# Optimization experiments

Hardware: AMD Instinct MI355X
Metric: run time of the kernel (lower is better)

Reference implementation:

```python
import jax, jax.numpy as jnp
import numpy as np

EMBED_DIM = 768
NUM_HEADS = 12
HEAD_DIM = EMBED_DIM // NUM_HEADS


def setup_inputs() -> dict:
    key = jax.random.key(0)
    k1, k2, k3, k4, k5 = jax.random.split(key, 5)
    x_q = jax.random.normal(k1, (8, 1024, EMBED_DIM), dtype=jnp.float32)
    s = 1.0 / np.sqrt(EMBED_DIM)
    qkv_w = jax.random.uniform(k2, (3 * EMBED_DIM, EMBED_DIM), jnp.float32, -s, s)
    qkv_b = jax.random.uniform(k3, (3 * EMBED_DIM,), jnp.float32, -s, s)
    out_w = jax.random.uniform(k4, (EMBED_DIM, EMBED_DIM), jnp.float32, -s, s)
    out_b = jax.random.uniform(k5, (EMBED_DIM,), jnp.float32, -s, s)
    return {"x_q": x_q, "qkv_w": qkv_w, "qkv_b": qkv_b, "out_w": out_w, "out_b": out_b}


def reference(x_q, qkv_w, qkv_b, out_w, out_b):
    b, p, c = x_q.shape
    scaling = HEAD_DIM ** (-0.5)
    # qkv projection: [b, p, 3c]
    qkv = x_q @ qkv_w.T + qkv_b
    qkv = qkv.reshape(b, p, 3, NUM_HEADS, HEAD_DIM)
    q = qkv[:, :, 0].transpose(0, 2, 1, 3) * scaling  # [b, h, p, d]
    k = qkv[:, :, 1].transpose(0, 2, 1, 3)
    v = qkv[:, :, 2].transpose(0, 2, 1, 3)
    attn = jnp.einsum('bhqd,bhkd->bhqk', q, k)
    attn = jax.nn.softmax(attn, axis=-1)
    out = jnp.einsum('bhqk,bhkd->bhqd', attn, v)
    out = out.transpose(0, 2, 1, 3).reshape(b, p, c)
    return out @ out_w.T + out_b
```

## Files before the change

kernel.cpp:

```cpp
#include <hip/hip_runtime.h>
#include <stdint.h>

typedef float  f32x4 __attribute__((ext_vector_type(4)));
typedef int    i32x4 __attribute__((ext_vector_type(4)));
typedef short  bf16x8 __attribute__((ext_vector_type(8)));
typedef unsigned short u16;
typedef unsigned int   u32;

#define DEVINL __device__ __forceinline__

DEVINL u16 f2bf(float f) {
  u32 u = __builtin_bit_cast(u32, f);
  u32 r = u + 0x7fffu + ((u >> 16) & 1u);
  return (u16)(r >> 16);
}

DEVINL u32 cvtpk(float lo, float hi) {
  u32 r;
  asm("v_cvt_pk_bf16_f32 %0, %1, %2" : "=v"(r) : "v"(lo), "v"(hi));
  return r;
}

DEVINL void mfma16(f32x4& d, i32x4 a, i32x4 b) {
  d = __builtin_amdgcn_mfma_f32_16x16x32_bf16(
      __builtin_bit_cast(bf16x8, a), __builtin_bit_cast(bf16x8, b), d, 0, 0, 0);
}

#define GLD16(gp, lp) __builtin_amdgcn_global_load_lds( \
    (__attribute__((address_space(1))) void*)(gp), \
    (__attribute__((address_space(3))) void*)(lp), 16, 0, 0)

__global__ void cvt3_f32_bf16(const float* __restrict__ s0, u16* __restrict__ d0, int n0,
                              const float* __restrict__ s1, u16* __restrict__ d1, int n1,
                              const float* __restrict__ s2, u16* __restrict__ d2, int n2) {
  int i = blockIdx.x * blockDim.x + threadIdx.x;
  int stride = gridDim.x * blockDim.x;
  int nt = n0 + n1 + n2;
  for (; i < nt; i += stride) {
    const float* s; u16* d; int j = i;
    if (j < n0) { s = s0; d = d0; }
    else if ((j -= n0) < n1) { s = s1; d = d1; }
    else { j -= n1; s = s2; d = d2; }
    float4 v = ((const float4*)s)[j];
    ushort4 o;
    o.x = f2bf(v.x); o.y = f2bf(v.y); o.z = f2bf(v.z); o.w = f2bf(v.w);
    ((ushort4*)d)[j] = o;
  }
}

template<int BM, int BN, int FM, int FN, int EPI>
__global__ __launch_bounds__(256) void gemm_bt(
    const u16* __restrict__ A, const u16* __restrict__ Bw,
    int M, int N, const float* __restrict__ bias,
    float* __restrict__ Cf, u16* __restrict__ Qb, u16* __restrict__ Kb, u16* __restrict__ Vtb)
{
  constexpr int BK = 32;
  constexpr int K  = 768;
  constexpr int ABYT = BM * BK * 2;
  constexpr int BBYT = BN * BK * 2;
  __shared__ __align__(16) unsigned char sm[2 * (ABYT + BBYT)];

  const int tid = threadIdx.x;
  const int l   = tid & 63;
  const int wid = tid >> 6;
  const int wm  = wid >> 1, wn = wid & 1;
  const int g4  = l >> 4;
  const int c15 = l & 15;

  const int ntiles = N / BN;
  const int wg  = ntiles * (M / BM);
  const int per = wg >> 3;
  const int tile = ((int)blockIdx.x & 7) * per + ((int)blockIdx.x >> 3);
  const int mbase = (tile / ntiles) * BM;
  const int nbase = (tile % ntiles) * BN;

  auto stage = [&](int buf, int kt) {
    unsigned char* ab = sm + buf * (ABYT + BBYT);
    unsigned char* bb = ab + ABYT;
    #pragma unroll
    for (int c = 0; c < BM / 64; ++c) {
      int ch = c * 256 + tid;
      int row = ch & (BM - 1), pl = ch / BM;
      GLD16(A + (size_t)(mbase + row) * K + kt * BK + pl * 8, ab + ch * 16);
    }
    #pragma unroll
    for (int c = 0; c < BN / 64; ++c) {
      int ch = c * 256 + tid;
      int row = ch & (BN - 1), pl = ch / BN;
      GLD16(Bw + (size_t)(nbase + row) * K + kt * BK + pl * 8, bb + ch * 16);
    }
  };

  f32x4 acc[FM][FN] = {};

  stage(0, 0);
  __syncthreads();

  for (int kt = 0; kt < K / BK; ++kt) {
    int cur = kt & 1;
    if (kt + 1 < K / BK) stage(cur ^ 1, kt + 1);
    unsigned char* ab = sm + cur * (ABYT + BBYT);
    unsigned char* bb = ab + ABYT;
    i32x4 af[FM], bf[FN];
    #pragma unroll
    for (int mt = 0; mt < FM; ++mt) {
      int row = wm * (BM / 2) + mt * 16 + c15;
      af[mt] = *(const i32x4*)(ab + (g4 * BM + row) * 16);
    }
    #pragma unroll
    for (int nt = 0; nt < FN; ++nt) {
      int row = wn * (BN / 2) + nt * 16 + c15;
      bf[nt] = *(const i32x4*)(bb + (g4 * BN + row) * 16);
    }
    __builtin_amdgcn_s_setprio(1);
    #pragma unroll
    for (int mt = 0; mt < FM; ++mt)
      #pragma unroll
      for (int nt = 0; nt < FN; ++nt)
        mfma16(acc[mt][nt], af[mt], bf[nt]);
    __builtin_amdgcn_s_setprio(0);
    __syncthreads();
  }

  if constexpr (EPI == 0) {
    #pragma unroll
    for (int nt = 0; nt < FN; ++nt) {
      int n = nbase + wn * (BN / 2) + nt * 16 + c15;
      float bv = bias[n];
      #pragma unroll
      for (int mt = 0; mt < FM; ++mt) {
        int m0 = mbase + wm * (BM / 2) + mt * 16 + g4 * 4;
        float* dst = Cf + (size_t)m0 * N + n;
        #pragma unroll
        for (int j = 0; j < 4; ++j) dst[(size_t)j * N] = acc[mt][nt][j] + bv;
      }
    }
  } else {
    #pragma unroll
    for (int nt = 0; nt < FN; ++nt) {
      int n = nbase + wn * (BN / 2) + nt * 16 + c15;
      int which = n / 768;
      int rem = n - which * 768;
      int h = rem >> 6, d = rem & 63;
      float bv = bias[n];
      #pragma unroll
      for (int mt = 0; mt < FM; ++mt) {
        int m0 = mbase + wm * (BM / 2) + mt * 16 + g4 * 4;
        int b = m0 >> 10, p0 = m0 & 1023;
        int bh = b * 12 + h;
        if (which == 0) {
          u16* dst = Qb + ((size_t)bh * 1024 + p0) * 64 + d;
          #pragma unroll
          for (int j = 0; j < 4; ++j) dst[(size_t)j * 64] = f2bf((acc[mt][nt][j] + bv) * 0.125f);
        } else if (which == 1) {
          u16* dst = Kb + ((size_t)bh * 1024 + p0) * 64 + d;
          #pragma unroll
          for (int j = 0; j < 4; ++j) dst[(size_t)j * 64] = f2bf(acc[mt][nt][j] + bv);
        } else {
          uint2 uu;
          uu.x = cvtpk(acc[mt][nt][0] + bv, acc[mt][nt][1] + bv);
          uu.y = cvtpk(acc[mt][nt][2] + bv, acc[mt][nt][3] + bv);
          *(uint2*)(Vtb + ((size_t)bh * 64 + d) * 1024 + p0) = uu;
        }
      }
    }
  }
}

__global__ __launch_bounds__(256) void attn_fwd(
    const u16* __restrict__ Qb, const u16* __restrict__ Kb,
    const u16* __restrict__ Vtb, u16* __restrict__ Ob)
{
  __shared__ __align__(16) unsigned char sm[16384 + 4 * 8192];
  const int tid = threadIdx.x;
  const int l = tid & 63, wid = tid >> 6;
  const int g4 = l >> 4, c15 = l & 15;
  const int bid = blockIdx.x;
  const int bh = bid % 96, qt = bid / 96;

  const size_t bhoff = (size_t)bh * (1024 * 64);
  const u16* Qg = Qb + bhoff + (size_t)qt * 128 * 64;
  const u16* Kg = Kb + bhoff;
  const u16* Vg = Vtb + bhoff;

  #pragma unroll
  for (int c = 0; c < 4; ++c) {
    int ch = c * 256 + tid;
    int row = ch & 127, pl = ch >> 7;
    GLD16(Qg + (size_t)row * 64 + pl * 8, sm + ch * 16);
  }

  auto stageKV = [&](int buf, int t) {
    unsigned char* kb_ = sm + 16384 + buf * 8192;
    unsigned char* vb_ = sm + 32768 + buf * 8192;
    #pragma unroll
    for (int c = 0; c < 2; ++c) {
      int ch = c * 256 + tid;
      int row = ch & 63, pl = ch >> 6;
      GLD16(Kg + (size_t)(t * 64 + row) * 64 + pl * 8, kb_ + ch * 16);
      GLD16(Vg + (size_t)row * 1024 + t * 64 + pl * 8, vb_ + ch * 16);
    }
  };

  stageKV(0, 0);
  __syncthreads();

  i32x4 qf[2][2];
  #pragma unroll
  for (int qn = 0; qn < 2; ++qn)
    #pragma unroll
    for (int ks = 0; ks < 2; ++ks) {
      int row = wid * 32 + qn * 16 + c15;
      qf[qn][ks] = *(const i32x4*)(sm + ((ks * 4 + g4) * 128 + row) * 16);
    }
  __syncthreads();

  unsigned char* pw = sm + wid * 4096;

  const i32x4 ones = {0x3F803F80, 0x3F803F80, 0x3F803F80, 0x3F803F80};
  constexpr float LOG2E = 1.44269504f;

  f32x4 ot[4][2] = {};
  f32x4 lacc[2] = {};
  float mrow[2] = {-1e30f, -1e30f};
  float mc[2]   = {-1e30f, -1e30f};

  for (int t = 0; t < 16; ++t) {
    int cur = t & 1;
    if (t + 1 < 16) stageKV(cur ^ 1, t + 1);
    unsigned char* kb_ = sm + 16384 + cur * 8192;
    unsigned char* vb_ = sm + 32768 + cur * 8192;

    f32x4 st[4][2] = {};
    __builtin_amdgcn_s_setprio(1);
    #pragma unroll
    for (int ks = 0; ks < 2; ++ks)
      #pragma unroll
      for (int kmt = 0; kmt < 4; ++kmt) {
        i32x4 ka = *(const i32x4*)(kb_ + ((ks * 4 + g4) * 64 + kmt * 16 + c15) * 16);
        mfma16(st[kmt][0], ka, qf[0][ks]);
        mfma16(st[kmt][1], ka, qf[1][ks]);
      }
    __builtin_amdgcn_s_setprio(0);

    #pragma unroll
    for (int qn = 0; qn < 2; ++qn) {
      float mx = fmaxf(fmaxf(fmaxf(st[0][qn][0], st[0][qn][1]), fmaxf(st[0][qn][2], st[0][qn][3])),
                       fmaxf(fmaxf(st[1][qn][0], st[1][qn][1]), fmaxf(st[1][qn][2], st[1][qn][3])));
      mx = fmaxf(mx,
           fmaxf(fmaxf(fmaxf(st[2][qn][0], st[2][qn][1]), fmaxf(st[2][qn][2], st[2][qn][3])),
                 fmaxf(fmaxf(st[3][qn][0], st[3][qn][1]), fmaxf(st[3][qn][2], st[3][qn][3]))));
      mx = fmaxf(mx, __shfl_xor(mx, 16));
      mx = fmaxf(mx, __shfl_xor(mx, 32));
      if (!__all(mx - mrow[qn] <= 8.0f)) {
        float mnew = fmaxf(mrow[qn], mx);
        float sfq = exp2f((mrow[qn] - mnew) * LOG2E);
        mrow[qn] = mnew;
        mc[qn] = mnew * LOG2E;
        #pragma unroll
        for (int dmt = 0; dmt < 4; ++dmt)
          #pragma unroll
          for (int j = 0; j < 4; ++j) ot[dmt][qn][j] *= sfq;
        lacc[qn][0] *= sfq;
      }
      #pragma unroll
      for (int kmt = 0; kmt < 4; ++kmt) {
        float p0 = exp2f(__builtin_fmaf(st[kmt][qn][0], LOG2E, -mc[qn]));
        float p1 = exp2f(__builtin_fmaf(st[kmt][qn][1], LOG2E, -mc[qn]));
        float p2 = exp2f(__builtin_fmaf(st[kmt][qn][2], LOG2E, -mc[qn]));
        float p3 = exp2f(__builtin_fmaf(st[kmt][qn][3], LOG2E, -mc[qn]));
        int k0 = kmt * 16 + 4 * g4;
        uint2 ww;
        ww.x = cvtpk(p0, p1);
        ww.y = cvtpk(p2, p3);
        *(uint2*)(pw + ((k0 >> 3) * 32 + qn * 16 + c15) * 16 + (k0 & 7) * 2) = ww;
      }
    }

    i32x4 pb[2][2];
    #pragma unroll
    for (int qn = 0; qn < 2; ++qn)
      #pragma unroll
      for (int ks = 0; ks < 2; ++ks)
        pb[qn][ks] = *(const i32x4*)(pw + (((ks * 4 + g4) * 32) + qn * 16 + c15) * 16);

    __builtin_amdgcn_s_setprio(1);
    #pragma unroll
    for (int ks = 0; ks < 2; ++ks) {
      #pragma unroll
      for (int dmt = 0; dmt < 4; ++dmt) {
        i32x4 va = *(const i32x4*)(vb_ + ((ks * 4 + g4) * 64 + dmt * 16 + c15) * 16);
        mfma16(ot[dmt][0], va, pb[0][ks]);
        mfma16(ot[dmt][1], va, pb[1][ks]);
      }
      mfma16(lacc[0], ones, pb[0][ks]);
      mfma16(lacc[1], ones, pb[1][ks]);
    }
    __builtin_amdgcn_s_setprio(0);
    __syncthreads();
  }

  const int b = bh / 12, h = bh % 12;
  #pragma unroll
  for (int qn = 0; qn < 2; ++qn) {
    float inv = 1.0f / lacc[qn][0];
    int q = qt * 128 + wid * 32 + qn * 16 + c15;
    size_t rowoff = ((size_t)(b * 1024 + q) * 12 + h) * 64;
    #pragma unroll
    for (int dmt = 0; dmt < 4; ++dmt) {
      int d0 = dmt * 16 + g4 * 4;
      uint2 uu;
      uu.x = cvtpk(ot[dmt][qn][0] * inv, ot[dmt][qn][1] * inv);
      uu.y = cvtpk(ot[dmt][qn][2] * inv, ot[dmt][qn][3] * inv);
      *(uint2*)(Ob + rowoff + d0) = uu;
    }
  }
}

extern "C" void kernel_launch(void* const* d_in, const int* in_sizes, int n_in,
                              void* d_out, int out_size, void* d_ws, size_t ws_size,
                              hipStream_t stream) {
  const float* x    = (const float*)d_in[0];
  const float* qkvw = (const float*)d_in[1];
  const float* qkvb = (const float*)d_in[2];
  const float* outw = (const float*)d_in[3];
  const float* outb = (const float*)d_in[4];
  float* out = (float*)d_out;

  unsigned char* ws = (unsigned char*)d_ws;
  u16* xb  = (u16*)(ws);
  u16* wqb = (u16*)(ws + 12582912);
  u16* wob = (u16*)(ws + 16121856);
  u16* Qbf = (u16*)(ws + 17301504);
  u16* Kbf = (u16*)(ws + 29884416);
  u16* Vtb = (u16*)(ws + 42467328);
  u16* Ob  = xb;

  cvt3_f32_bf16<<<dim3(2048), dim3(256), 0, stream>>>(
      x, xb, 8192 * 768 / 4, qkvw, wqb, 2304 * 768 / 4, outw, wob, 768 * 768 / 4);

  gemm_bt<128, 128, 4, 4, 1><<<dim3(1152), dim3(256), 0, stream>>>(
      xb, wqb, 8192, 2304, qkvb, nullptr, Qbf, Kbf, Vtb);

  attn_fwd<<<dim3(768), dim3(256), 0, stream>>>(Qbf, Kbf, Vtb, Ob);

  gemm_bt<128, 64, 4, 2, 0><<<dim3(768), dim3(256), 0, stream>>>(
      Ob, wob, 8192, 768, outb, out, nullptr, nullptr, nullptr);
}
```

Before: 175.7 us.

## Replace QKV GEMM with 256x256-tile 8-wave kernel and split-phase pipeline

Replaces the 128x128 QKV projection GEMM with a dedicated 512-thread kernel that computes 256x256 output tiles using BK=64, double-buffered 128KB LDS, and a four-phase schedule per k-step. Each phase interleaves register loads from LDS, half-tile async prefetches of the next step and MFMA bursts, using explicit barriers and vmcnt waits. The larger tile raises arithmetic intensity and cuts global reloads of A and B. The cost is one block per CU with 288 blocks on 256 CUs, which leaves a partial second wave, plus high register pressure from 128 accumulator floats per thread. The output-projection GEMM template drops its unused QKV epilogue.

```diff
diff --git a/kernel.cpp b/kernel.cpp
--- a/kernel.cpp
+++ b/kernel.cpp
@@ -29,6 +29,10 @@
 #define GLD16(gp, lp) __builtin_amdgcn_global_load_lds( \
     (__attribute__((address_space(1))) void*)(gp), \
     (__attribute__((address_space(3))) void*)(lp), 16, 0, 0)
+
+#define VMW(n) do { asm volatile("s_waitcnt vmcnt(" #n ")" ::: "memory"); \
+                    __builtin_amdgcn_sched_barrier(0); } while (0)
+#define BAR() __builtin_amdgcn_s_barrier()
 
 __global__ void cvt3_f32_bf16(const float* __restrict__ s0, u16* __restrict__ d0, int n0,
                               const float* __restrict__ s1, u16* __restrict__ d1, int n1,
@@ -48,11 +52,176 @@
   }
 }
 
-template<int BM, int BN, int FM, int FN, int EPI>
+__global__ __launch_bounds__(512) void gemm_qkv_8p(
+    const u16* __restrict__ A, const u16* __restrict__ Bw,
+    const float* __restrict__ bias,
+    u16* __restrict__ Qb, u16* __restrict__ Kb, u16* __restrict__ Vtb)
+{
+  constexpr int K = 768, T = 12;
+  __shared__ __align__(16) unsigned char sm[131072];
+  unsigned char* smA = sm;
+  unsigned char* smB = sm + 65536;
+
+  const int tid = threadIdx.x;
+  const int l   = tid & 63;
+  const int wid = tid >> 6;
+  const int wm  = wid >> 2, wn = wid & 3;
+  const int g4  = l >> 4;
+  const int c15 = l & 15;
+
+  constexpr int ntiles = 9;
+  const int tile = ((int)blockIdx.x & 7) * 36 + ((int)blockIdx.x >> 3);
+  const int mbase = (tile / ntiles) * 256;
+  const int nbase = (tile % ntiles) * 256;
+
+  auto stA = [&](int bb, int kt, int h) {
+    #pragma unroll
+    for (int p = 0; p < 2; ++p) {
+      int ch = p * 512 + tid;
+      int row = ch & 127, pl = ch >> 7;
+      GLD16(A + (size_t)(mbase + h * 128 + row) * K + kt * 64 + pl * 8,
+            smA + bb * 32768 + (pl * 256 + h * 128 + row) * 16);
+    }
+  };
+  auto stB = [&](int bb, int kt, int h) {
+    #pragma unroll
+    for (int p = 0; p < 2; ++p) {
+      int ch = p * 512 + tid;
+      int row = ch & 127, pl = ch >> 7;
+      GLD16(Bw + (size_t)(nbase + h * 128 + row) * K + kt * 64 + pl * 8,
+            smB + bb * 32768 + (pl * 256 + h * 128 + row) * 16);
+    }
+  };
+
+  f32x4 acc[8][4] = {};
+  i32x4 a[4][2], bq[2][2];
+
+  stA(0, 0, 0); stB(0, 0, 0); stB(0, 0, 1); stA(0, 0, 1);
+  __syncthreads();
+
+  for (int t = 0; t < T; ++t) {
+    const int cur = t & 1, nxt = cur ^ 1;
+    const bool pf = (t + 1 < T);
+    unsigned char* cA = smA + cur * 32768;
+    unsigned char* cB = smB + cur * 32768;
+
+    #pragma unroll
+    for (int i = 0; i < 4; ++i)
+      #pragma unroll
+      for (int ks = 0; ks < 2; ++ks)
+        a[i][ks] = *(const i32x4*)(cA + ((ks * 4 + g4) * 256 + wm * 128 + i * 16 + c15) * 16);
+    #pragma unroll
+    for (int j = 0; j < 2; ++j)
+      #pragma unroll
+      for (int ks = 0; ks < 2; ++ks)
+        bq[j][ks] = *(const i32x4*)(cB + ((ks * 4 + g4) * 256 + wn * 64 + j * 16 + c15) * 16);
+    if (pf) { stA(nxt, t + 1, 0); stB(nxt, t + 1, 0); }
+    BAR();
+    __builtin_amdgcn_s_setprio(1);
+    #pragma unroll
+    for (int i = 0; i < 4; ++i)
+      #pragma unroll
+      for (int j = 0; j < 2; ++j)
+        #pragma unroll
+        for (int ks = 0; ks < 2; ++ks)
+          mfma16(acc[i][j], a[i][ks], bq[j][ks]);
+    __builtin_amdgcn_s_setprio(0);
+    BAR();
+
+    #pragma unroll
+    for (int j = 0; j < 2; ++j)
+      #pragma unroll
+      for (int ks = 0; ks < 2; ++ks)
+        bq[j][ks] = *(const i32x4*)(cB + ((ks * 4 + g4) * 256 + wn * 64 + 32 + j * 16 + c15) * 16);
+    if (pf) { stA(nxt, t + 1, 1); stB(nxt, t + 1, 1); }
+    BAR();
+    __builtin_amdgcn_s_setprio(1);
+    #pragma unroll
+    for (int i = 0; i < 4; ++i)
+      #pragma unroll
+      for (int j = 0; j < 2; ++j)
+        #pragma unroll
+        for (int ks = 0; ks < 2; ++ks)
+          mfma16(acc[i][2 + j], a[i][ks], bq[j][ks]);
+    __builtin_amdgcn_s_setprio(0);
+    BAR();
+
+    #pragma unroll
+    for (int i = 0; i < 4; ++i)
+      #pragma unroll
+      for (int ks = 0; ks < 2; ++ks)
+        a[i][ks] = *(const i32x4*)(cA + ((ks * 4 + g4) * 256 + wm * 128 + 64 + i * 16 + c15) * 16);
+    #pragma unroll
+    for (int j = 0; j < 2; ++j)
+      #pragma unroll
+      for (int ks = 0; ks < 2; ++ks)
+        bq[j][ks] = *(const i32x4*)(cB + ((ks * 4 + g4) * 256 + wn * 64 + j * 16 + c15) * 16);
+    BAR();
+    __builtin_amdgcn_s_setprio(1);
+    #pragma unroll
+    for (int i = 0; i < 4; ++i)
+      #pragma unroll
+      for (int j = 0; j < 2; ++j)
+        #pragma unroll
+        for (int ks = 0; ks < 2; ++ks)
+          mfma16(acc[4 + i][j], a[i][ks], bq[j][ks]);
+    __builtin_amdgcn_s_setprio(0);
+    if (pf) { VMW(4); }
+    BAR();
+
+    #pragma unroll
+    for (int j = 0; j < 2; ++j)
+      #pragma unroll
+      for (int ks = 0; ks < 2; ++ks)
+        bq[j][ks] = *(const i32x4*)(cB + ((ks * 4 + g4) * 256 + wn * 64 + 32 + j * 16 + c15) * 16);
+    BAR();
+    __builtin_amdgcn_s_setprio(1);
+    #pragma unroll
+    for (int i = 0; i < 4; ++i)
+      #pragma unroll
+      for (int j = 0; j < 2; ++j)
+        #pragma unroll
+        for (int ks = 0; ks < 2; ++ks)
+          mfma16(acc[4 + i][2 + j], a[i][ks], bq[j][ks]);
+    __builtin_amdgcn_s_setprio(0);
+    if (pf) { VMW(0); }
+    BAR();
+  }
+
+  #pragma unroll
+  for (int nj = 0; nj < 4; ++nj) {
+    int n = nbase + wn * 64 + nj * 16 + c15;
+    int which = n / 768;
+    int rem = n - which * 768;
+    int h = rem >> 6, d = rem & 63;
+    float bv = bias[n];
+    #pragma unroll
+    for (int mi = 0; mi < 8; ++mi) {
+      int m0 = mbase + wm * 128 + mi * 16 + g4 * 4;
+      int b = m0 >> 10, p0 = m0 & 1023;
+      int bh = b * 12 + h;
+      if (which == 0) {
+        u16* dst = Qb + ((size_t)bh * 1024 + p0) * 64 + d;
+        #pragma unroll
+        for (int jj = 0; jj < 4; ++jj) dst[(size_t)jj * 64] = f2bf((acc[mi][nj][jj] + bv) * 0.125f);
+      } else if (which == 1) {
+        u16* dst = Kb + ((size_t)bh * 1024 + p0) * 64 + d;
+        #pragma unroll
+        for (int jj = 0; jj < 4; ++jj) dst[(size_t)jj * 64] = f2bf(acc[mi][nj][jj] + bv);
+      } else {
+        uint2 uu;
+        uu.x = cvtpk(acc[mi][nj][0] + bv, acc[mi][nj][1] + bv);
+        uu.y = cvtpk(acc[mi][nj][2] + bv, acc[mi][nj][3] + bv);
+        *(uint2*)(Vtb + ((size_t)bh * 64 + d) * 1024 + p0) = uu;
+      }
+    }
+  }
+}
+
+template<int BM, int BN, int FM, int FN>
 __global__ __launch_bounds__(256) void gemm_bt(
     const u16* __restrict__ A, const u16* __restrict__ Bw,
-    int M, int N, const float* __restrict__ bias,
-    float* __restrict__ Cf, u16* __restrict__ Qb, u16* __restrict__ Kb, u16* __restrict__ Vtb)
+    int M, int N, const float* __restrict__ bias, float* __restrict__ Cf)
 {
   constexpr int BK = 32;
   constexpr int K  = 768;
@@ -122,47 +291,16 @@
     __syncthreads();
   }
 
-  if constexpr (EPI == 0) {
-    #pragma unroll
-    for (int nt = 0; nt < FN; ++nt) {
-      int n = nbase + wn * (BN / 2) + nt * 16 + c15;
-      float bv = bias[n];
-      #pragma unroll
-      for (int mt = 0; mt < FM; ++mt) {
-        int m0 = mbase + wm * (BM / 2) + mt * 16 + g4 * 4;
-        float* dst = Cf + (size_t)m0 * N + n;
-        #pragma unroll
-        for (int j = 0; j < 4; ++j) dst[(size_t)j * N] = acc[mt][nt][j] + bv;
-      }
-    }
-  } else {
-    #pragma unroll
-    for (int nt = 0; nt < FN; ++nt) {
-      int n = nbase + wn * (BN / 2) + nt * 16 + c15;
-      int which = n / 768;
-      int rem = n - which * 768;
-      int h = rem >> 6, d = rem & 63;
-      float bv = bias[n];
-      #pragma unroll
-      for (int mt = 0; mt < FM; ++mt) {
-        int m0 = mbase + wm * (BM / 2) + mt * 16 + g4 * 4;
-        int b = m0 >> 10, p0 = m0 & 1023;
-        int bh = b * 12 + h;
-        if (which == 0) {
-          u16* dst = Qb + ((size_t)bh * 1024 + p0) * 64 + d;
-          #pragma unroll
-          for (int j = 0; j < 4; ++j) dst[(size_t)j * 64] = f2bf((acc[mt][nt][j] + bv) * 0.125f);
-        } else if (which == 1) {
-          u16* dst = Kb + ((size_t)bh * 1024 + p0) * 64 + d;
-          #pragma unroll
-          for (int j = 0; j < 4; ++j) dst[(size_t)j * 64] = f2bf(acc[mt][nt][j] + bv);
-        } else {
-          uint2 uu;
-          uu.x = cvtpk(acc[mt][nt][0] + bv, acc[mt][nt][1] + bv);
-          uu.y = cvtpk(acc[mt][nt][2] + bv, acc[mt][nt][3] + bv);
-          *(uint2*)(Vtb + ((size_t)bh * 64 + d) * 1024 + p0) = uu;
-        }
-      }
+  #pragma unroll
+  for (int nt = 0; nt < FN; ++nt) {
+    int n = nbase + wn * (BN / 2) + nt * 16 + c15;
+    float bv = bias[n];
+    #pragma unroll
+    for (int mt = 0; mt < FM; ++mt) {
+      int m0 = mbase + wm * (BM / 2) + mt * 16 + g4 * 4;
+      float* dst = Cf + (size_t)m0 * N + n;
+      #pragma unroll
+      for (int j = 0; j < 4; ++j) dst[(size_t)j * N] = acc[mt][nt][j] + bv;
     }
   }
 }
@@ -339,11 +477,11 @@
   cvt3_f32_bf16<<<dim3(2048), dim3(256), 0, stream>>>(
       x, xb, 8192 * 768 / 4, qkvw, wqb, 2304 * 768 / 4, outw, wob, 768 * 768 / 4);
 
-  gemm_bt<128, 128, 4, 4, 1><<<dim3(1152), dim3(256), 0, stream>>>(
-      xb, wqb, 8192, 2304, qkvb, nullptr, Qbf, Kbf, Vtb);
+  gemm_qkv_8p<<<dim3(288), dim3(512), 0, stream>>>(
+      xb, wqb, qkvb, Qbf, Kbf, Vtb);
 
   attn_fwd<<<dim3(768), dim3(256), 0, stream>>>(Qbf, Kbf, Vtb, Ob);
 
-  gemm_bt<128, 64, 4, 2, 0><<<dim3(768), dim3(256), 0, stream>>>(
-      Ob, wob, 8192, 768, outb, out, nullptr, nullptr, nullptr);
-}
+  gemm_bt<128, 64, 4, 2><<<dim3(768), dim3(256), 0, stream>>>(
+      Ob, wob, 8192, 768, outb, out);
+}
```

Measured after the change: 191.3 us. 1.09x slower.

## Triple-buffer GEMM k-loop with explicit vmcnt waits and split barriers

Applied to the files above, without the earlier changes.

Moves the bf16 GEMM from a double-buffered to a triple-buffered LDS pipeline with a prefetch distance of two k-tiles. Each tile's global-to-LDS copy is issued after that iteration's fragment reads. Explicit s_waitcnt vmcnt plus a raw s_barrier replace __syncthreads, so loads for the next tile can stay in flight across the barrier. This is meant to hide global memory latency, at the cost of more LDS per block (possibly lower occupancy) and fragile hand-coded wait counts.

```diff
diff --git a/kernel.cpp b/kernel.cpp
--- a/kernel.cpp
+++ b/kernel.cpp
@@ -29,6 +29,17 @@
 #define GLD16(gp, lp) __builtin_amdgcn_global_load_lds( \
     (__attribute__((address_space(1))) void*)(gp), \
     (__attribute__((address_space(3))) void*)(lp), 16, 0, 0)
+
+#define BAR() do { __builtin_amdgcn_s_barrier(); \
+                   __builtin_amdgcn_sched_barrier(0); } while (0)
+
+template<int N> DEVINL void vmwait() {
+  static_assert(N == 0 || N == 3 || N == 4, "literal vmcnt only");
+  if constexpr (N == 0) asm volatile("s_waitcnt vmcnt(0)" ::: "memory");
+  else if constexpr (N == 3) asm volatile("s_waitcnt vmcnt(3)" ::: "memory");
+  else                       asm volatile("s_waitcnt vmcnt(4)" ::: "memory");
+  __builtin_amdgcn_sched_barrier(0);
+}
 
 __global__ void cvt3_f32_bf16(const float* __restrict__ s0, u16* __restrict__ d0, int n0,
                               const float* __restrict__ s1, u16* __restrict__ d1, int n1,
@@ -56,9 +67,12 @@
 {
   constexpr int BK = 32;
   constexpr int K  = 768;
+  constexpr int T  = K / BK;
   constexpr int ABYT = BM * BK * 2;
   constexpr int BBYT = BN * BK * 2;
-  __shared__ __align__(16) unsigned char sm[2 * (ABYT + BBYT)];
+  constexpr int BUF  = ABYT + BBYT;
+  constexpr int NL   = (BM + BN) / 64;
+  __shared__ __align__(16) unsigned char sm[3 * BUF];
 
   const int tid = threadIdx.x;
   const int l   = tid & 63;
@@ -75,7 +89,7 @@
   const int nbase = (tile % ntiles) * BN;
 
   auto stage = [&](int buf, int kt) {
-    unsigned char* ab = sm + buf * (ABYT + BBYT);
+    unsigned char* ab = sm + buf * BUF;
     unsigned char* bb = ab + ABYT;
     #pragma unroll
     for (int c = 0; c < BM / 64; ++c) {
@@ -94,12 +108,13 @@
   f32x4 acc[FM][FN] = {};
 
   stage(0, 0);
-  __syncthreads();
-
-  for (int kt = 0; kt < K / BK; ++kt) {
-    int cur = kt & 1;
-    if (kt + 1 < K / BK) stage(cur ^ 1, kt + 1);
-    unsigned char* ab = sm + cur * (ABYT + BBYT);
+  stage(1, 1);
+  vmwait<NL>();
+  BAR();
+
+  int cb = 0, sb = 2;
+  for (int t = 0; t < T; ++t) {
+    unsigned char* ab = sm + cb * BUF;
     unsigned char* bb = ab + ABYT;
     i32x4 af[FM], bf[FN];
     #pragma unroll
@@ -112,6 +127,7 @@
       int row = wn * (BN / 2) + nt * 16 + c15;
       bf[nt] = *(const i32x4*)(bb + (g4 * BN + row) * 16);
     }
+    if (t + 2 < T) stage(sb, t + 2);
     __builtin_amdgcn_s_setprio(1);
     #pragma unroll
     for (int mt = 0; mt < FM; ++mt)
@@ -119,7 +135,11 @@
       for (int nt = 0; nt < FN; ++nt)
         mfma16(acc[mt][nt], af[mt], bf[nt]);
     __builtin_amdgcn_s_setprio(0);
-    __syncthreads();
+    if (t < T - 2)       vmwait<NL>();
+    else if (t == T - 2) vmwait<0>();
+    if (t + 1 < T) BAR();
+    cb = (cb == 2) ? 0 : cb + 1;
+    sb = (sb == 2) ? 0 : sb + 1;
   }
 
   if constexpr (EPI == 0) {
@@ -151,11 +171,11 @@
         if (which == 0) {
           u16* dst = Qb + ((size_t)bh * 1024 + p0) * 64 + d;
           #pragma unroll
-          for (int j = 0; j < 4; ++j) dst[(size_t)j * 64] = f2bf((acc[mt][nt][j] + bv) * 0.125f);
+          for (int jj = 0; jj < 4; ++jj) dst[(size_t)jj * 64] = f2bf((acc[mt][nt][jj] + bv) * 0.125f);
         } else if (which == 1) {
           u16* dst = Kb + ((size_t)bh * 1024 + p0) * 64 + d;
           #pragma unroll
-          for (int j = 0; j < 4; ++j) dst[(size_t)j * 64] = f2bf(acc[mt][nt][j] + bv);
+          for (int jj = 0; jj < 4; ++jj) dst[(size_t)jj * 64] = f2bf(acc[mt][nt][jj] + bv);
         } else {
           uint2 uu;
           uu.x = cvtpk(acc[mt][nt][0] + bv, acc[mt][nt][1] + bv);
```

New measurement: 179.1 us. About the same (+1.9%).
